# Kernel tuning notes

Hardware: AMD Instinct MI355X
Metric: run time of the kernel (lower is better)

## Reference

```python
import jax, jax.numpy as jnp
import numpy as np

N_NODES = 256
IN_FEATURES = 4096
OUT_FEATURES = 7
LAYERS = 4
WIRES = 8                      # ceil(log2(n_nodes))
DIM = 2 ** WIRES               # state-vector length = 256
P2 = WIRES * (WIRES - 1) // 2  # 28 controlled gates per block
N_W = 6 * WIRES + 3 * P2       # 132 weights per layer (matches weight_shape)
CPLX = jnp.complex64
# op2_all_layers ordering: gaps 1..w-1, then j
PAIRS = [(j, j + gap) for gap in range(1, WIRES) for j in range(WIRES - gap)]


def _ry(t):
    c, s = jnp.cos(t / 2), jnp.sin(t / 2)
    return jnp.stack([jnp.stack([c, -s]), jnp.stack([s, c])]).astype(CPLX)


def _rx(t):
    c = jnp.cos(t / 2).astype(CPLX)
    s = (-1j * jnp.sin(t / 2)).astype(CPLX)
    return jnp.stack([jnp.stack([c, s]), jnp.stack([s, c])])


def _rz(t):
    z = jnp.zeros((), CPLX)
    return jnp.stack([jnp.stack([jnp.exp(-0.5j * t).astype(CPLX), z]),
                      jnp.stack([z, jnp.exp(0.5j * t).astype(CPLX)])])


# Constant-angle gates (the source passes the integer weight index as the
# controlled-rotation angle, so these are compile-time numpy constants).
def _ry_np(a):
    c, s = np.cos(a / 2), np.sin(a / 2)
    return np.array([[c, -s], [s, c]], np.complex64)


def _rx_np(a):
    c, s = np.cos(a / 2), np.sin(a / 2)
    return np.array([[c, -1j * s], [-1j * s, c]], np.complex64)


def _rz_np(a):
    return np.diag([np.exp(-0.5j * a), np.exp(0.5j * a)]).astype(np.complex64)


def apply_1q(state, M, q):
    # state: [B] + [2]*WIRES; wire q lives on axis q+1 (wire 0 = MSB, PennyLane order)
    s = jnp.moveaxis(state, q + 1, -1)
    s = jnp.einsum('...b,ab->...a', s, M)
    return jnp.moveaxis(s, -1, q + 1)


def apply_c1q(state, M, c, t):
    # controlled gate: apply M on target wire t in the control==1 subspace
    s = jnp.moveaxis(state, (c + 1, t + 1), (-2, -1))
    s1 = jnp.einsum('...b,ab->...a', s[..., 1, :], M)
    s = jnp.stack([s[..., 0, :], s1], axis=-2)
    return jnp.moveaxis(s, (-2, -1), (c + 1, t + 1))


def q_layer(state, wv):
    # Faithful port of the source q_layer, including the quirk that the
    # CRY/CRX/CRZ angles are the integer running weight index (constants).
    wi = 0
    for q in range(WIRES):
        state = apply_1q(state, _ry(wv[wi + q]), q)
    wi += WIRES
    for i, (c, t) in enumerate(PAIRS):
        state = apply_c1q(state, _ry_np(float(wi + i)), c, t)
    wi += P2
    for q in range(WIRES):
        state = apply_1q(state, _ry(wv[wi + q]), q)
    wi += WIRES
    for q in range(WIRES):
        state = apply_1q(state, _rx(wv[wi + q]), q)
    wi += WIRES
    for i, (c, t) in enumerate(PAIRS):
        state = apply_c1q(state, _rx_np(float(wi + i)), c, t)
    wi += P2
    for q in range(WIRES):
        state = apply_1q(state, _rx(wv[wi + q]), q)
    wi += WIRES
    for q in range(WIRES):
        state = apply_1q(state, _rz(wv[wi + q]), q)
    wi += WIRES
    for i, (c, t) in enumerate(PAIRS):
        state = apply_c1q(state, _rz_np(float(wi + i)), c, t)
    wi += P2
    for q in range(WIRES):
        state = apply_1q(state, _rz(wv[wi + q]), q)
    return state


def circuit(samples, qweights):
    # samples: [B, N_NODES] real -> AmplitudeEmbedding(pad_with=0, normalize=True)
    B = samples.shape[0]
    v = samples
    if DIM > N_NODES:
        v = jnp.pad(v, ((0, 0), (0, DIM - N_NODES)))
    v = v / jnp.linalg.norm(v, axis=1, keepdims=True)
    state = v.astype(CPLX).reshape((B,) + (2,) * WIRES)
    layer = jax.checkpoint(q_layer)  # bounds residual memory under AD
    for l in range(LAYERS):
        state = layer(state, qweights[l])
    p = state.real ** 2 + state.imag ** 2  # probabilities, [B] + [2]*WIRES
    zs = []
    for q in range(WIRES):
        axes = tuple(a for a in range(1, WIRES + 1) if a != q + 1)
        m = p.sum(axis=axes)            # [B, 2]
        zs.append(m[:, 0] - m[:, 1])    # <Z_q> = P(0) - P(1)
    return jnp.stack(zs, axis=1)        # [B, WIRES]


def setup_inputs() -> dict:
    key = jax.random.key(0)
    k1, k2, k3, k4 = jax.random.split(key, 4)
    x = jax.random.normal(k1, (N_NODES, IN_FEATURES), jnp.float32)
    qweights = jax.random.uniform(k2, (LAYERS, N_W), jnp.float32, 0.0, 2.0 * np.pi)
    fc_w = jax.random.normal(k3, (OUT_FEATURES, WIRES), jnp.float32) / np.sqrt(WIRES)
    fc_b = jax.random.normal(k4, (OUT_FEATURES,), jnp.float32) / np.sqrt(WIRES)
    return {"x": x, "qweights": qweights, "fc_w": fc_w, "fc_b": fc_b}


def reference(x, qweights, fc_w, fc_b):
    z = circuit(x.T, qweights)      # [IN_FEATURES, WIRES]
    return z @ fc_w.T + fc_b        # [IN_FEATURES, OUT_FEATURES]
```

## Files before the change

kernel.cpp:

```cpp
#include <hip/hip_runtime.h>
#include <math.h>


namespace {

constexpr int NSAMP = 4096;
constexpr int NW_L  = 132;

constexpr double PI_D   = 3.14159265358979323846264338327950288;
constexpr double TWO_PI = 6.28318530717958647692528676655900577;

constexpr double red_pm_pi(double x) {
  double k = x / TWO_PI;
  long long ki = (long long)k;
  double r = x - (double)ki * TWO_PI;
  if (r > PI_D)  r -= TWO_PI;
  if (r < -PI_D) r += TWO_PI;
  return r;
}
constexpr double csin(double x) {
  double r = red_pm_pi(x), r2 = r * r, term = r, sum = r;
  for (int n = 1; n <= 13; ++n) { term *= -r2 / (double)((2*n)*(2*n+1)); sum += term; }
  return sum;
}
constexpr double ccos(double x) {
  double r = red_pm_pi(x), r2 = r * r, term = 1.0, sum = 1.0;
  for (int n = 1; n <= 13; ++n) { term *= -r2 / (double)((2*n-1)*(2*n)); sum += term; }
  return sum;
}

constexpr int PC[28] = {0,1,2,3,4,5,6, 0,1,2,3,4,5, 0,1,2,3,4, 0,1,2,3, 0,1,2, 0,1, 0};
constexpr int PT[28] = {1,2,3,4,5,6,7, 2,3,4,5,6,7, 3,4,5,6,7, 4,5,6,7, 5,6,7, 6,7, 7};

struct Tbl28 { float c[28]; float s[28]; };
constexpr Tbl28 mk_tbl(int base) {
  Tbl28 t{};
  for (int i = 0; i < 28; ++i) {
    double a = 0.5 * (double)(base + i);
    t.c[i] = (float)ccos(a);
    t.s[i] = (float)csin(a);
  }
  return t;
}
constexpr Tbl28 T_CRY = mk_tbl(8);
constexpr Tbl28 T_CRX = mk_tbl(52);

struct DTbl { float v[512]; };
constexpr DTbl mk_dcrz() {
  DTbl t{};
  for (int s = 0; s < 256; ++s) {
    double psi = 0.0;
    for (int i = 0; i < 28; ++i) {
      const int pc = 7 - PC[i], pt = 7 - PT[i];
      if ((s >> pc) & 1) {
        const double half = 0.5 * (double)(96 + i);
        psi += ((s >> pt) & 1) ? half : -half;
      }
    }
    t.v[2*s]   = (float)ccos(psi);
    t.v[2*s+1] = (float)csin(psi);
  }
  return t;
}
__device__ constexpr DTbl D_CRZ = mk_dcrz();

__device__ __forceinline__ float shx(float v, int sh) {
  if (sh == 0) {
    int r = __builtin_amdgcn_update_dpp((int)__float_as_uint(v), (int)__float_as_uint(v),
                                        0xB1, 0xF, 0xF, true);
    return __uint_as_float((unsigned)r);
  }
  if (sh == 1) {
    int r = __builtin_amdgcn_update_dpp((int)__float_as_uint(v), (int)__float_as_uint(v),
                                        0x4E, 0xF, 0xF, true);
    return __uint_as_float((unsigned)r);
  }
  return __shfl_xor(v, 1 << sh, 64);
}

__device__ __forceinline__ void gen_cross(float* ar, float* ai, int lane, int sh,
                                          float m00r, float m00i, float m01r, float m01i) {
  const int bbit = (lane >> sh) & 1;
  const float dr = m00r;
  const float di = bbit ? -m00i : m00i;
  const float g  = bbit ? -m01r : m01r;
  const float h  = m01i;
#pragma unroll
  for (int r = 0; r < 4; ++r) {
    float pr = shx(ar[r], sh);
    float pi = shx(ai[r], sh);
    float mr = ar[r], mi = ai[r];
    ar[r] = dr*mr - di*mi + g*pr - h*pi;
    ai[r] = dr*mi + di*mr + g*pi + h*pr;
  }
}
__device__ __forceinline__ void gen_local(float* ar, float* ai, int p,
                                          float m00r, float m00i, float m01r, float m01i) {
  const int m = 1 << p;
#pragma unroll
  for (int r0 = 0; r0 < 4; ++r0) {
    if (!(r0 & m)) {
      const int r1 = r0 | m;
      float a0r=ar[r0], a0i=ai[r0], a1r=ar[r1], a1i=ai[r1];
      ar[r0] =  m00r*a0r - m00i*a0i + m01r*a1r - m01i*a1i;
      ai[r0] =  m00r*a0i + m00i*a0r + m01r*a1i + m01i*a1r;
      ar[r1] = -m01r*a0r - m01i*a0i + m00r*a1r + m00i*a1i;
      ai[r1] = -m01r*a0i + m01i*a0r + m00r*a1i - m00i*a1r;
    }
  }
}
__device__ __forceinline__ void cry_cross(float* ar, float* ai, int lane,
                                          int shc, int sht, float cc, float sc) {
  const int ctrl = (lane >> shc) & 1;
  const float ce = ctrl ? cc : 1.0f;
  float se = ((lane >> sht) & 1) ? sc : -sc;
  se = ctrl ? se : 0.0f;
#pragma unroll
  for (int r = 0; r < 4; ++r) {
    float pr = shx(ar[r], sht);
    float pi = shx(ai[r], sht);
    ar[r] = ce*ar[r] + se*pr;
    ai[r] = ce*ai[r] + se*pi;
  }
}
__device__ __forceinline__ void cry_local(float* ar, float* ai, int lane,
                                          int shc, int pt, float cc, float sc) {
  const int ctrl = (lane >> shc) & 1;
  const float ce = ctrl ? cc : 1.0f;
  const float se = ctrl ? sc : 0.0f;
  const int m = 1 << pt;
#pragma unroll
  for (int r0 = 0; r0 < 4; ++r0) {
    if (!(r0 & m)) {
      const int r1 = r0 | m;
      float a0r=ar[r0], a0i=ai[r0], a1r=ar[r1], a1i=ai[r1];
      ar[r0] = ce*a0r - se*a1r;  ai[r0] = ce*a0i - se*a1i;
      ar[r1] = ce*a1r + se*a0r;  ai[r1] = ce*a1i + se*a0i;
    }
  }
}
__device__ __forceinline__ void ry_pair23(float* ar, float* ai, float cc, float sc) {
  float a0r=ar[2], a0i=ai[2], a1r=ar[3], a1i=ai[3];
  ar[2] = cc*a0r - sc*a1r;  ai[2] = cc*a0i - sc*a1i;
  ar[3] = cc*a1r + sc*a0r;  ai[3] = cc*a1i + sc*a0i;
}
__device__ __forceinline__ void crx_cross(float* ar, float* ai, int lane,
                                          int shc, int sht, float cc, float sc) {
  const int ctrl = (lane >> shc) & 1;
  const float ce = ctrl ? cc : 1.0f;
  const float se = ctrl ? sc : 0.0f;
#pragma unroll
  for (int r = 0; r < 4; ++r) {
    float pr = shx(ar[r], sht);
    float pi = shx(ai[r], sht);
    ar[r] = ce*ar[r] + se*pi;
    ai[r] = ce*ai[r] - se*pr;
  }
}
__device__ __forceinline__ void crx_local(float* ar, float* ai, int lane,
                                          int shc, int pt, float cc, float sc) {
  const int ctrl = (lane >> shc) & 1;
  const float ce = ctrl ? cc : 1.0f;
  const float se = ctrl ? sc : 0.0f;
  const int m = 1 << pt;
#pragma unroll
  for (int r0 = 0; r0 < 4; ++r0) {
    if (!(r0 & m)) {
      const int r1 = r0 | m;
      float a0r=ar[r0], a0i=ai[r0], a1r=ar[r1], a1i=ai[r1];
      ar[r0] = ce*a0r + se*a1i;  ai[r0] = ce*a0i - se*a1r;
      ar[r1] = ce*a1r + se*a0i;  ai[r1] = ce*a1i - se*a0r;
    }
  }
}
__device__ __forceinline__ void rx_pair23(float* ar, float* ai, float cc, float sc) {
  float a0r=ar[2], a0i=ai[2], a1r=ar[3], a1i=ai[3];
  ar[2] = cc*a0r + sc*a1i;  ai[2] = cc*a0i - sc*a1r;
  ar[3] = cc*a1r + sc*a0i;  ai[3] = cc*a1i - sc*a0r;
}

__device__ __forceinline__ unsigned short f2bf(float f) {
  unsigned int u = __float_as_uint(f);
  u = (u + 0x7FFFu + ((u >> 16) & 1u)) >> 16;
  return (unsigned short)u;
}

typedef __attribute__((ext_vector_type(8))) short bf16x8;
typedef __attribute__((ext_vector_type(4))) float f32x4;

}

__global__ __launch_bounds__(64) void build_emit(const float* __restrict__ qw,
                                                 unsigned short* __restrict__ U1bf,
                                                 unsigned short* __restrict__ W2bf) {
  __shared__ float4 sM[48];
  const int lane = threadIdx.x;
  const int h    = blockIdx.x >> 8;
  const int s0   = blockIdx.x & 255;

  if (lane < 48) {
    const int lp  = lane / 24;
    const int rem = lane - lp * 24;
    const int j   = rem >> 3;
    const int q   = rem & 7;
    const int l   = 2 * h + lp;
    float a, bb;
    if (j == 0) {
      a  = qw[l * NW_L + q];
      bb = (l > 0) ? qw[(l - 1) * NW_L + 124 + q] : 0.f;
    } else if (j == 1) {
      a  = qw[l * NW_L + 44 + q];
      bb = qw[l * NW_L + 36 + q];
    } else {
      a  = (l < 3) ? qw[l * NW_L + 88 + q] : 0.f;
      bb = qw[l * NW_L + 80 + q];
    }
    float sa, ca, sb, cb;
    __sincosf(0.5f * a,  &sa, &ca);
    __sincosf(0.5f * bb, &sb, &cb);
    float4 m;
    if (j == 0)      m = make_float4(ca*cb, -ca*sb, -sa*cb, -sa*sb);
    else if (j == 1) m = make_float4(ca*cb, -sa*sb, -ca*sb, -sa*cb);
    else             m = make_float4(ca*cb, -sa*cb, -sb*sa, -sb*ca);
    sM[lane] = m;
  }

  float ar[4], ai[4];
#pragma unroll
  for (int r = 0; r < 4; ++r) {
    ar[r] = (((lane << 2) | r) == s0) ? 1.f : 0.f;
    ai[r] = 0.f;
  }
  float dzr[4], dzi[4];
#pragma unroll
  for (int r = 0; r < 4; ++r) {
    const int s = (lane << 2) | r;
    dzr[r] = D_CRZ.v[2*s];
    dzi[r] = D_CRZ.v[2*s+1];
  }
  __syncthreads();

#pragma unroll 1
  for (int lp = 0; lp < 2; ++lp) {
    const int base = lp * 24;
#pragma unroll
    for (int q = 0; q < 8; ++q) {
      float4 m = sM[base + q];
      if (q <= 5) gen_cross(ar, ai, lane, 5 - q, m.x, m.y, m.z, m.w);
      else        gen_local(ar, ai, 7 - q, m.x, m.y, m.z, m.w);
    }
#pragma unroll
    for (int i = 0; i < 28; ++i) {
      const int c = PC[i], t = PT[i];
      const float cc = T_CRY.c[i], sc = T_CRY.s[i];
      if (t <= 5)      cry_cross(ar, ai, lane, 5 - c, 5 - t, cc, sc);
      else if (c <= 5) cry_local(ar, ai, lane, 5 - c, 7 - t, cc, sc);
      else             ry_pair23(ar, ai, cc, sc);
    }
#pragma unroll
    for (int q = 0; q < 8; ++q) {
      float4 m = sM[base + 8 + q];
      if (q <= 5) gen_cross(ar, ai, lane, 5 - q, m.x, m.y, m.z, m.w);
      else        gen_local(ar, ai, 7 - q, m.x, m.y, m.z, m.w);
    }
#pragma unroll
    for (int i = 0; i < 28; ++i) {
      const int c = PC[i], t = PT[i];
      const float cc = T_CRX.c[i], sc = T_CRX.s[i];
      if (t <= 5)      crx_cross(ar, ai, lane, 5 - c, 5 - t, cc, sc);
      else if (c <= 5) crx_local(ar, ai, lane, 5 - c, 7 - t, cc, sc);
      else             rx_pair23(ar, ai, cc, sc);
    }
#pragma unroll
    for (int q = 0; q < 8; ++q) {
      float4 m = sM[base + 16 + q];
      if (q <= 5) gen_cross(ar, ai, lane, 5 - q, m.x, m.y, m.z, m.w);
      else        gen_local(ar, ai, 7 - q, m.x, m.y, m.z, m.w);
    }
    if (2 * h + lp < 3) {
#pragma unroll
      for (int r = 0; r < 4; ++r) {
        float mr = ar[r], mi = ai[r];
        ar[r] = mr*dzr[r] - mi*dzi[r];
        ai[r] = mr*dzi[r] + mi*dzr[r];
      }
    }
  }

  if (h == 0) {
#pragma unroll
    for (int r = 0; r < 4; ++r) {
      const int o = (lane << 2) | r;
      U1bf[(size_t)o * 256 + s0]         = f2bf(ar[r]);
      U1bf[(size_t)(o + 256) * 256 + s0] = f2bf(ai[r]);
    }
  } else {
#pragma unroll
    for (int r = 0; r < 4; ++r) {
      const int o = (lane << 2) | r;
      W2bf[(size_t)o * 512 + s0]               = f2bf(ar[r]);
      W2bf[(size_t)(o + 256) * 512 + s0]       = f2bf(ai[r]);
      W2bf[(size_t)o * 512 + 256 + s0]         = f2bf(-ai[r]);
      W2bf[(size_t)(o + 256) * 512 + 256 + s0] = f2bf(ar[r]);
    }
  }
}

__global__ __launch_bounds__(1024) void eval_chain(const float* __restrict__ x,
                                                   const unsigned short* __restrict__ U1bf,
                                                   const unsigned short* __restrict__ W2bf,
                                                   const float* __restrict__ fcw,
                                                   const float* __restrict__ fcb,
                                                   float* __restrict__ out) {
  __shared__ unsigned short Xs[16 * 264];
  __shared__ unsigned short Ys[16 * 520];
  __shared__ float Zp[16][16][9];
  __shared__ float Zf[16][9];
  const int tid  = threadIdx.x;
  const int lane = tid & 63;
  const int w    = tid >> 6;
  const int colbase = blockIdx.x * 16;

  {
    const int k  = tid >> 2;
    const int c4 = (tid & 3) * 4;
    const float4 v = *(const float4*)(x + (size_t)k * NSAMP + colbase + c4);
    Xs[(c4 + 0) * 264 + k] = f2bf(v.x);
    Xs[(c4 + 1) * 264 + k] = f2bf(v.y);
    Xs[(c4 + 2) * 264 + k] = f2bf(v.z);
    Xs[(c4 + 3) * 264 + k] = f2bf(v.w);
  }
  __syncthreads();

  const int quad = lane >> 4;
  const int n    = lane & 15;
  const int rowb = w * 32;

  {
    f32x4 a1[2];
    a1[0] = (f32x4){0.f, 0.f, 0.f, 0.f};
    a1[1] = (f32x4){0.f, 0.f, 0.f, 0.f};
#pragma unroll
    for (int kt = 0; kt < 8; ++kt) {
      const bf16x8 bfrag = *(const bf16x8*)&Xs[n * 264 + kt * 32 + quad * 8];
#pragma unroll
      for (int rt = 0; rt < 2; ++rt) {
        const int row = rowb + rt * 16 + n;
        const bf16x8 afrag = *(const bf16x8*)(U1bf + (size_t)row * 256 + kt * 32 + quad * 8);
        a1[rt] = __builtin_amdgcn_mfma_f32_16x16x32_bf16(afrag, bfrag, a1[rt], 0, 0, 0);
      }
    }
#pragma unroll
    for (int rt = 0; rt < 2; ++rt) {
      unsigned short p4[4];
#pragma unroll
      for (int reg = 0; reg < 4; ++reg) p4[reg] = f2bf(a1[rt][reg]);
      *(uint2*)&Ys[n * 520 + rowb + rt * 16 + quad * 4] = *(const uint2*)p4;
    }
  }
  __syncthreads();

  f32x4 acc[2];
  acc[0] = (f32x4){0.f, 0.f, 0.f, 0.f};
  acc[1] = (f32x4){0.f, 0.f, 0.f, 0.f};
#pragma unroll
  for (int kt = 0; kt < 16; ++kt) {
    const bf16x8 bfrag = *(const bf16x8*)&Ys[n * 520 + kt * 32 + quad * 8];
#pragma unroll
    for (int rt = 0; rt < 2; ++rt) {
      const int row = rowb + rt * 16 + n;
      const bf16x8 afrag = *(const bf16x8*)(W2bf + (size_t)row * 512 + kt * 32 + quad * 8);
      acc[rt] = __builtin_amdgcn_mfma_f32_16x16x32_bf16(afrag, bfrag, acc[rt], 0, 0, 0);
    }
  }

  float za[9];
#pragma unroll
  for (int i = 0; i < 9; ++i) za[i] = 0.f;
  const float m4 = (lane & 32) ? -1.f : 1.f;
  const float m5 = (lane & 16) ? -1.f : 1.f;
#pragma unroll
  for (int rt = 0; rt < 2; ++rt) {
#pragma unroll
    for (int reg = 0; reg < 4; ++reg) {
      const float v = acc[rt][reg];
      const float p = v * v;
      za[0] += p;
      za[1] += (w & 4)   ? -p : p;
      za[2] += (w & 2)   ? -p : p;
      za[3] += (w & 1)   ? -p : p;
      za[4] += rt        ? -p : p;
      za[5] = fmaf(m4, p, za[5]);
      za[6] = fmaf(m5, p, za[6]);
      za[7] += (reg & 2) ? -p : p;
      za[8] += (reg & 1) ? -p : p;
    }
  }
#pragma unroll
  for (int off = 16; off <= 32; off <<= 1) {
#pragma unroll
    for (int i = 0; i < 9; ++i) za[i] += __shfl_xor(za[i], off, 64);
  }
  if (lane < 16) {
#pragma unroll
    for (int i = 0; i < 9; ++i) Zp[w][lane][i] = za[i];
  }
  __syncthreads();

  if (tid < 144) {
    const int col = tid / 9, q = tid - col * 9;
    float z = 0.f;
#pragma unroll
    for (int ww = 0; ww < 16; ++ww) z += Zp[ww][col][q];
    Zf[col][q] = z;
  }
  __syncthreads();

  if (tid < 112) {
    const int col = tid / 7, oo = tid - col * 7;
    const float inv = 1.f / Zf[col][0];
    float v = fcb[oo];
#pragma unroll
    for (int q = 0; q < 8; ++q)
      v = fmaf(fcw[oo * 8 + q], Zf[col][1 + q] * inv, v);
    out[(size_t)(colbase + col) * 7 + oo] = v;
  }
}

extern "C" void kernel_launch(void* const* d_in, const int* in_sizes, int n_in,
                              void* d_out, int out_size, void* d_ws, size_t ws_size,
                              hipStream_t stream) {
  const float* x   = (const float*)d_in[0];
  const float* qw  = (const float*)d_in[1];
  const float* fcw = (const float*)d_in[2];
  const float* fcb = (const float*)d_in[3];
  float* out = (float*)d_out;

  unsigned short* U1bf = (unsigned short*)d_ws;
  unsigned short* W2bf = U1bf + (size_t)512 * 256;

  hipLaunchKernelGGL(build_emit, dim3(512), dim3(64),   0, stream, qw, U1bf, W2bf);
  hipLaunchKernelGGL(eval_chain, dim3(256), dim3(1024), 0, stream,
                     x, U1bf, W2bf, fcw, fcb, out);
}
```

Baseline: 100.8 us.

## Build unitary rows via adjoint circuit to enable coalesced vector stores

Rather than propagating basis vectors forward to get unitary columns, each block now applies the inverse (adjoint) circuit to a basis vector, which yields a conjugated row of the unitary. The gates run in reverse order with negated off-diagonal and sine terms, and the result is conjugated when written. Each lane can then write four contiguous bf16 values as a single 8-byte store, replacing the strided scalar stores with a 256- or 512-element stride. This depends on the adjoint sign conventions being exactly right for every gate type.

```diff
diff --git a/kernel.cpp b/kernel.cpp
--- a/kernel.cpp
+++ b/kernel.cpp
@@ -190,13 +190,13 @@
 
 }
 
-__global__ __launch_bounds__(64) void build_emit(const float* __restrict__ qw,
+__global__ __launch_bounds__(64) void build_rows(const float* __restrict__ qw,
                                                  unsigned short* __restrict__ U1bf,
                                                  unsigned short* __restrict__ W2bf) {
   __shared__ float4 sM[48];
   const int lane = threadIdx.x;
   const int h    = blockIdx.x >> 8;
-  const int s0   = blockIdx.x & 255;
+  const int o    = blockIdx.x & 255;
 
   if (lane < 48) {
     const int lp  = lane / 24;
@@ -228,7 +228,7 @@
   float ar[4], ai[4];
 #pragma unroll
   for (int r = 0; r < 4; ++r) {
-    ar[r] = (((lane << 2) | r) == s0) ? 1.f : 0.f;
+    ar[r] = (((lane << 2) | r) == o) ? 1.f : 0.f;
     ai[r] = 0.f;
   }
   float dzr[4], dzi[4];
@@ -236,48 +236,15 @@
   for (int r = 0; r < 4; ++r) {
     const int s = (lane << 2) | r;
     dzr[r] = D_CRZ.v[2*s];
-    dzi[r] = D_CRZ.v[2*s+1];
+    dzi[r] = -D_CRZ.v[2*s+1];
   }
   __syncthreads();
 
 #pragma unroll 1
-  for (int lp = 0; lp < 2; ++lp) {
+  for (int lp = 1; lp >= 0; --lp) {
+    const int l    = 2 * h + lp;
     const int base = lp * 24;
-#pragma unroll
-    for (int q = 0; q < 8; ++q) {
-      float4 m = sM[base + q];
-      if (q <= 5) gen_cross(ar, ai, lane, 5 - q, m.x, m.y, m.z, m.w);
-      else        gen_local(ar, ai, 7 - q, m.x, m.y, m.z, m.w);
-    }
-#pragma unroll
-    for (int i = 0; i < 28; ++i) {
-      const int c = PC[i], t = PT[i];
-      const float cc = T_CRY.c[i], sc = T_CRY.s[i];
-      if (t <= 5)      cry_cross(ar, ai, lane, 5 - c, 5 - t, cc, sc);
-      else if (c <= 5) cry_local(ar, ai, lane, 5 - c, 7 - t, cc, sc);
-      else             ry_pair23(ar, ai, cc, sc);
-    }
-#pragma unroll
-    for (int q = 0; q < 8; ++q) {
-      float4 m = sM[base + 8 + q];
-      if (q <= 5) gen_cross(ar, ai, lane, 5 - q, m.x, m.y, m.z, m.w);
-      else        gen_local(ar, ai, 7 - q, m.x, m.y, m.z, m.w);
-    }
-#pragma unroll
-    for (int i = 0; i < 28; ++i) {
-      const int c = PC[i], t = PT[i];
-      const float cc = T_CRX.c[i], sc = T_CRX.s[i];
-      if (t <= 5)      crx_cross(ar, ai, lane, 5 - c, 5 - t, cc, sc);
-      else if (c <= 5) crx_local(ar, ai, lane, 5 - c, 7 - t, cc, sc);
-      else             rx_pair23(ar, ai, cc, sc);
-    }
-#pragma unroll
-    for (int q = 0; q < 8; ++q) {
-      float4 m = sM[base + 16 + q];
-      if (q <= 5) gen_cross(ar, ai, lane, 5 - q, m.x, m.y, m.z, m.w);
-      else        gen_local(ar, ai, 7 - q, m.x, m.y, m.z, m.w);
-    }
-    if (2 * h + lp < 3) {
+    if (l < 3) {
 #pragma unroll
       for (int r = 0; r < 4; ++r) {
         float mr = ar[r], mi = ai[r];
@@ -285,24 +252,58 @@
         ai[r] = mr*dzi[r] + mi*dzr[r];
       }
     }
-  }
-
+#pragma unroll
+    for (int q = 0; q < 8; ++q) {
+      float4 m = sM[base + 16 + q];
+      if (q <= 5) gen_cross(ar, ai, lane, 5 - q, m.x, -m.y, -m.z, -m.w);
+      else        gen_local(ar, ai, 7 - q, m.x, -m.y, -m.z, -m.w);
+    }
+#pragma unroll
+    for (int i = 27; i >= 0; --i) {
+      const int c = PC[i], t = PT[i];
+      const float cc = T_CRX.c[i], sc = -T_CRX.s[i];
+      if (t <= 5)      crx_cross(ar, ai, lane, 5 - c, 5 - t, cc, sc);
+      else if (c <= 5) crx_local(ar, ai, lane, 5 - c, 7 - t, cc, sc);
+      else             rx_pair23(ar, ai, cc, sc);
+    }
+#pragma unroll
+    for (int q = 0; q < 8; ++q) {
+      float4 m = sM[base + 8 + q];
+      if (q <= 5) gen_cross(ar, ai, lane, 5 - q, m.x, -m.y, -m.z, -m.w);
+      else        gen_local(ar, ai, 7 - q, m.x, -m.y, -m.z, -m.w);
+    }
+#pragma unroll
+    for (int i = 27; i >= 0; --i) {
+      const int c = PC[i], t = PT[i];
+      const float cc = T_CRY.c[i], sc = -T_CRY.s[i];
+      if (t <= 5)      cry_cross(ar, ai, lane, 5 - c, 5 - t, cc, sc);
+      else if (c <= 5) cry_local(ar, ai, lane, 5 - c, 7 - t, cc, sc);
+      else             ry_pair23(ar, ai, cc, sc);
+    }
+#pragma unroll
+    for (int q = 0; q < 8; ++q) {
+      float4 m = sM[base + q];
+      if (q <= 5) gen_cross(ar, ai, lane, 5 - q, m.x, -m.y, -m.z, -m.w);
+      else        gen_local(ar, ai, 7 - q, m.x, -m.y, -m.z, -m.w);
+    }
+  }
+
+  unsigned short re4[4], im4[4], ni4[4];
+#pragma unroll
+  for (int r = 0; r < 4; ++r) {
+    re4[r] = f2bf(ar[r]);
+    im4[r] = f2bf(-ai[r]);
+    ni4[r] = f2bf(ai[r]);
+  }
+  const int off = lane * 4;
   if (h == 0) {
-#pragma unroll
-    for (int r = 0; r < 4; ++r) {
-      const int o = (lane << 2) | r;
-      U1bf[(size_t)o * 256 + s0]         = f2bf(ar[r]);
-      U1bf[(size_t)(o + 256) * 256 + s0] = f2bf(ai[r]);
-    }
+    *(uint2*)(U1bf + (size_t)o * 256 + off)         = *(const uint2*)re4;
+    *(uint2*)(U1bf + (size_t)(o + 256) * 256 + off) = *(const uint2*)im4;
   } else {
-#pragma unroll
-    for (int r = 0; r < 4; ++r) {
-      const int o = (lane << 2) | r;
-      W2bf[(size_t)o * 512 + s0]               = f2bf(ar[r]);
-      W2bf[(size_t)(o + 256) * 512 + s0]       = f2bf(ai[r]);
-      W2bf[(size_t)o * 512 + 256 + s0]         = f2bf(-ai[r]);
-      W2bf[(size_t)(o + 256) * 512 + 256 + s0] = f2bf(ar[r]);
-    }
+    *(uint2*)(W2bf + (size_t)o * 512 + off)               = *(const uint2*)re4;
+    *(uint2*)(W2bf + (size_t)o * 512 + 256 + off)         = *(const uint2*)ni4;
+    *(uint2*)(W2bf + (size_t)(o + 256) * 512 + off)       = *(const uint2*)im4;
+    *(uint2*)(W2bf + (size_t)(o + 256) * 512 + 256 + off) = *(const uint2*)re4;
   }
 }
 
@@ -439,7 +440,7 @@
   unsigned short* U1bf = (unsigned short*)d_ws;
   unsigned short* W2bf = U1bf + (size_t)512 * 256;
 
-  hipLaunchKernelGGL(build_emit, dim3(512), dim3(64),   0, stream, qw, U1bf, W2bf);
+  hipLaunchKernelGGL(build_rows, dim3(512), dim3(64),   0, stream, qw, U1bf, W2bf);
   hipLaunchKernelGGL(eval_chain, dim3(256), dim3(1024), 0, stream,
                      x, U1bf, W2bf, fcw, fcb, out);
 }
```

Result: no change. 99.56 us (-1.2%).

## Build per-layer unitaries in parallel and combine pairs with complex GEMM

Applied to the files above, without the earlier changes.

The previous build kernel simulated two layers serially per basis column to form each two-layer unitary. Now each of the four layer unitaries is built by its own block (1024 blocks, one layer each), stored in fp32, and a new combine kernel multiplies adjacent pairs with a tiled complex GEMM before emitting the bf16 U1/W2 matrices. This halves the serial gate chain per block and raises parallelism, at the cost of an extra launch, 2 MB of fp32 workspace traffic, and the GEMM work.

```diff
diff --git a/kernel.cpp b/kernel.cpp
--- a/kernel.cpp
+++ b/kernel.cpp
@@ -188,22 +188,48 @@
 typedef __attribute__((ext_vector_type(8))) short bf16x8;
 typedef __attribute__((ext_vector_type(4))) float f32x4;
 
-}
-
-__global__ __launch_bounds__(64) void build_emit(const float* __restrict__ qw,
-                                                 unsigned short* __restrict__ U1bf,
-                                                 unsigned short* __restrict__ W2bf) {
-  __shared__ float4 sM[48];
+__device__ __forceinline__ void cgemm_tile(const float* __restrict__ bufA,
+                                           const float* __restrict__ bufB,
+                                           int bi, int bj, int tid,
+                                           float& accr, float& acci,
+                                           float2* S2 , float2* S1 ) {
+  const int ti = tid & 15;
+  const int tj = tid >> 4;
+  accr = 0.f; acci = 0.f;
+#pragma unroll 1
+  for (int kt = 0; kt < 8; ++kt) {
+    __syncthreads();
+#pragma unroll
+    for (int v = 0; v < 2; ++v) {
+      const int s = v * 256 + tid;
+      const int k = s >> 4, i = s & 15;
+      S2[k * 16 + i] = *(const float2*)(bufA + (size_t)(kt*32 + k) * 512 + (bi*16 + i) * 2);
+      const int j2 = s >> 5, k2 = s & 31;
+      S1[j2 * 33 + k2] = *(const float2*)(bufB + (size_t)(bj*16 + j2) * 512 + (kt*32 + k2) * 2);
+    }
+    __syncthreads();
+#pragma unroll
+    for (int kk = 0; kk < 32; ++kk) {
+      const float2 a = S2[kk * 16 + ti];
+      const float2 b = S1[tj * 33 + kk];
+      accr = fmaf(a.x, b.x, accr);  accr = fmaf(-a.y, b.y, accr);
+      acci = fmaf(a.x, b.y, acci);  acci = fmaf(a.y, b.x, acci);
+    }
+  }
+}
+
+}
+
+__global__ __launch_bounds__(64) void build_quarter(const float* __restrict__ qw,
+                                                    float* __restrict__ Uq) {
+  __shared__ float4 sM[24];
   const int lane = threadIdx.x;
-  const int h    = blockIdx.x >> 8;
+  const int l    = blockIdx.x >> 8;
   const int s0   = blockIdx.x & 255;
 
-  if (lane < 48) {
-    const int lp  = lane / 24;
-    const int rem = lane - lp * 24;
-    const int j   = rem >> 3;
-    const int q   = rem & 7;
-    const int l   = 2 * h + lp;
+  if (lane < 24) {
+    const int j = lane >> 3;
+    const int q = lane & 7;
     float a, bb;
     if (j == 0) {
       a  = qw[l * NW_L + q];
@@ -240,69 +266,98 @@
   }
   __syncthreads();
 
-#pragma unroll 1
-  for (int lp = 0; lp < 2; ++lp) {
-    const int base = lp * 24;
-#pragma unroll
-    for (int q = 0; q < 8; ++q) {
-      float4 m = sM[base + q];
-      if (q <= 5) gen_cross(ar, ai, lane, 5 - q, m.x, m.y, m.z, m.w);
-      else        gen_local(ar, ai, 7 - q, m.x, m.y, m.z, m.w);
-    }
-#pragma unroll
-    for (int i = 0; i < 28; ++i) {
-      const int c = PC[i], t = PT[i];
-      const float cc = T_CRY.c[i], sc = T_CRY.s[i];
-      if (t <= 5)      cry_cross(ar, ai, lane, 5 - c, 5 - t, cc, sc);
-      else if (c <= 5) cry_local(ar, ai, lane, 5 - c, 7 - t, cc, sc);
-      else             ry_pair23(ar, ai, cc, sc);
-    }
-#pragma unroll
-    for (int q = 0; q < 8; ++q) {
-      float4 m = sM[base + 8 + q];
-      if (q <= 5) gen_cross(ar, ai, lane, 5 - q, m.x, m.y, m.z, m.w);
-      else        gen_local(ar, ai, 7 - q, m.x, m.y, m.z, m.w);
-    }
-#pragma unroll
-    for (int i = 0; i < 28; ++i) {
-      const int c = PC[i], t = PT[i];
-      const float cc = T_CRX.c[i], sc = T_CRX.s[i];
-      if (t <= 5)      crx_cross(ar, ai, lane, 5 - c, 5 - t, cc, sc);
-      else if (c <= 5) crx_local(ar, ai, lane, 5 - c, 7 - t, cc, sc);
-      else             rx_pair23(ar, ai, cc, sc);
-    }
-#pragma unroll
-    for (int q = 0; q < 8; ++q) {
-      float4 m = sM[base + 16 + q];
-      if (q <= 5) gen_cross(ar, ai, lane, 5 - q, m.x, m.y, m.z, m.w);
-      else        gen_local(ar, ai, 7 - q, m.x, m.y, m.z, m.w);
-    }
-    if (2 * h + lp < 3) {
-#pragma unroll
-      for (int r = 0; r < 4; ++r) {
-        float mr = ar[r], mi = ai[r];
-        ar[r] = mr*dzr[r] - mi*dzi[r];
-        ai[r] = mr*dzi[r] + mi*dzr[r];
-      }
-    }
-  }
-
-  if (h == 0) {
+#pragma unroll
+  for (int q = 0; q < 8; ++q) {
+    float4 m = sM[q];
+    if (q <= 5) gen_cross(ar, ai, lane, 5 - q, m.x, m.y, m.z, m.w);
+    else        gen_local(ar, ai, 7 - q, m.x, m.y, m.z, m.w);
+  }
+#pragma unroll
+  for (int i = 0; i < 28; ++i) {
+    const int c = PC[i], t = PT[i];
+    const float cc = T_CRY.c[i], sc = T_CRY.s[i];
+    if (t <= 5)      cry_cross(ar, ai, lane, 5 - c, 5 - t, cc, sc);
+    else if (c <= 5) cry_local(ar, ai, lane, 5 - c, 7 - t, cc, sc);
+    else             ry_pair23(ar, ai, cc, sc);
+  }
+#pragma unroll
+  for (int q = 0; q < 8; ++q) {
+    float4 m = sM[8 + q];
+    if (q <= 5) gen_cross(ar, ai, lane, 5 - q, m.x, m.y, m.z, m.w);
+    else        gen_local(ar, ai, 7 - q, m.x, m.y, m.z, m.w);
+  }
+#pragma unroll
+  for (int i = 0; i < 28; ++i) {
+    const int c = PC[i], t = PT[i];
+    const float cc = T_CRX.c[i], sc = T_CRX.s[i];
+    if (t <= 5)      crx_cross(ar, ai, lane, 5 - c, 5 - t, cc, sc);
+    else if (c <= 5) crx_local(ar, ai, lane, 5 - c, 7 - t, cc, sc);
+    else             rx_pair23(ar, ai, cc, sc);
+  }
+#pragma unroll
+  for (int q = 0; q < 8; ++q) {
+    float4 m = sM[16 + q];
+    if (q <= 5) gen_cross(ar, ai, lane, 5 - q, m.x, m.y, m.z, m.w);
+    else        gen_local(ar, ai, 7 - q, m.x, m.y, m.z, m.w);
+  }
+  if (l < 3) {
 #pragma unroll
     for (int r = 0; r < 4; ++r) {
-      const int o = (lane << 2) | r;
-      U1bf[(size_t)o * 256 + s0]         = f2bf(ar[r]);
-      U1bf[(size_t)(o + 256) * 256 + s0] = f2bf(ai[r]);
+      float mr = ar[r], mi = ai[r];
+      ar[r] = mr*dzr[r] - mi*dzi[r];
+      ai[r] = mr*dzi[r] + mi*dzr[r];
+    }
+  }
+
+  float4* dst = (float4*)(Uq + (size_t)(l * 256 + s0) * 512);
+  dst[2*lane]     = make_float4(ar[0], ai[0], ar[1], ai[1]);
+  dst[2*lane + 1] = make_float4(ar[2], ai[2], ar[3], ai[3]);
+}
+
+__global__ __launch_bounds__(256) void combine_emit(const float* __restrict__ Uq,
+                                                    unsigned short* __restrict__ U1bf,
+                                                    unsigned short* __restrict__ W2bf) {
+  __shared__ float2 S2[32 * 16];
+  __shared__ float2 S1[16 * 33];
+  __shared__ float Tre[16][17];
+  __shared__ float Tim[16][17];
+  const int tid = threadIdx.x;
+  const int p   = blockIdx.x >> 8;
+  const int rem = blockIdx.x & 255;
+  const int bi  = rem & 15;
+  const int bj  = rem >> 4;
+  const float* bufA = Uq + (size_t)(2*p + 1) * 256 * 512;
+  const float* bufB = Uq + (size_t)(2*p) * 256 * 512;
+
+  float accr, acci;
+  cgemm_tile(bufA, bufB, bi, bj, tid, accr, acci, S2, S1);
+
+  Tre[tid & 15][tid >> 4] = accr;
+  Tim[tid & 15][tid >> 4] = acci;
+  __syncthreads();
+
+  const int part = tid >> 6;
+  const int rr   = (tid & 63) >> 2;
+  const int cg   = tid & 3;
+  unsigned short pk[4];
+  if (p == 0) {
+    if (part < 2) {
+#pragma unroll
+      for (int k = 0; k < 4; ++k)
+        pk[k] = f2bf(part ? Tim[rr][cg*4 + k] : Tre[rr][cg*4 + k]);
+      const int row = bi * 16 + rr + part * 256;
+      *(uint2*)(U1bf + (size_t)row * 256 + bj * 16 + cg * 4) = *(const uint2*)pk;
     }
   } else {
 #pragma unroll
-    for (int r = 0; r < 4; ++r) {
-      const int o = (lane << 2) | r;
-      W2bf[(size_t)o * 512 + s0]               = f2bf(ar[r]);
-      W2bf[(size_t)(o + 256) * 512 + s0]       = f2bf(ai[r]);
-      W2bf[(size_t)o * 512 + 256 + s0]         = f2bf(-ai[r]);
-      W2bf[(size_t)(o + 256) * 512 + 256 + s0] = f2bf(ar[r]);
-    }
+    for (int k = 0; k < 4; ++k) {
+      const float v = (part == 0 || part == 3) ? Tre[rr][cg*4 + k]
+                    : (part == 1 ? -Tim[rr][cg*4 + k] : Tim[rr][cg*4 + k]);
+      pk[k] = f2bf(v);
+    }
+    const int row = bi * 16 + rr + ((part >= 2) ? 256 : 0);
+    const int col = bj * 16 + cg * 4 + ((part & 1) ? 256 : 0);
+    *(uint2*)(W2bf + (size_t)row * 512 + col) = *(const uint2*)pk;
   }
 }
 
@@ -436,10 +491,12 @@
   const float* fcb = (const float*)d_in[3];
   float* out = (float*)d_out;
 
-  unsigned short* U1bf = (unsigned short*)d_ws;
+  float* Uq = (float*)d_ws;
+  unsigned short* U1bf = (unsigned short*)(Uq + (size_t)4 * 256 * 512);
   unsigned short* W2bf = U1bf + (size_t)512 * 256;
 
-  hipLaunchKernelGGL(build_emit, dim3(512), dim3(64),   0, stream, qw, U1bf, W2bf);
-  hipLaunchKernelGGL(eval_chain, dim3(256), dim3(1024), 0, stream,
+  hipLaunchKernelGGL(build_quarter, dim3(1024), dim3(64),   0, stream, qw, Uq);
+  hipLaunchKernelGGL(combine_emit,  dim3(512),  dim3(256),  0, stream, Uq, U1bf, W2bf);
+  hipLaunchKernelGGL(eval_chain,    dim3(256),  dim3(1024), 0, stream,
                      x, U1bf, W2bf, fcw, fcb, out);
 }
```

Result: slower. 104.5 us (+3.7%).
